# Performance work log

Measured on AMD Instinct MI355X. Metric: run time of the kernel, lower is better.

Reference implementation:

```python
import jax, jax.numpy as jnp
import numpy as np

N = 4096
D_IN = 1024
D_Q = 1024
D_V = 1024

def setup_inputs() -> dict:
    key = jax.random.key(0)
    ks = jax.random.split(key, 8)
    # x scaled down a bit so exp() of raw (unstable, no max-subtract) scores stays finite,
    # matching the original module's numerics regime.
    x = jax.random.normal(ks[0], (N, D_IN), dtype=jnp.float32) * 0.02
    mask = jax.random.uniform(ks[1], (N, N), dtype=jnp.float32)
    s = 1.0 / np.sqrt(D_IN)
    Wq = jax.random.normal(ks[2], (D_IN, D_Q), dtype=jnp.float32) * s
    bq = jax.random.normal(ks[3], (D_Q,), dtype=jnp.float32) * 0.02
    Wk = jax.random.normal(ks[4], (D_IN, D_Q), dtype=jnp.float32) * s
    bk = jax.random.normal(ks[5], (D_Q,), dtype=jnp.float32) * 0.02
    Wv = jax.random.normal(ks[6], (D_IN, D_V), dtype=jnp.float32) * s
    bv = jax.random.normal(ks[7], (D_V,), dtype=jnp.float32) * 0.02
    return {"x": x, "mask": mask, "Wq": Wq, "bq": bq, "Wk": Wk, "bk": bk, "Wv": Wv, "bv": bv}

def reference(x, mask, Wq, bq, Wk, bk, Wv, bv):
    # Q, K, V projections (nn.Linear: x @ W + b, here W stored as [in, out])
    Q = x @ Wq + bq          # [N, Dq]
    K = x @ Wk + bk          # [N, Dq]
    V = x @ Wv + bv          # [N, Dv]
    scale = 1.0              # default scale in original forward
    scores = scale * (Q @ K.T)   # [N, N]
    scores = mask * scores       # elementwise multiplicative mask
    # Faithful to original (quirky) normalization:
    # exp(S) / sum(exp(S), axis=1)[None, :]  -> row-sums broadcast across ROWS
    e = jnp.exp(scores)                       # [N, N]
    denom = jnp.sum(e, axis=1)[None, :]       # [1, N]
    softmax = e / denom                       # [N, N]
    return softmax @ V                        # [N, Dv]
```

## Files before the change

### kernel.cpp

```cpp
#include <hip/hip_runtime.h>
#include <hip/hip_bf16.h>


#define N_TOK 4096
#define D_DIM 1024

typedef __bf16 bf16x8 __attribute__((ext_vector_type(8)));
typedef __bf16 bf16x4 __attribute__((ext_vector_type(4)));
typedef float  f32x4  __attribute__((ext_vector_type(4)));

typedef const __attribute__((address_space(1))) char g_char;
typedef __attribute__((address_space(3))) char lds_char;

__global__ void cvt_f32_to_bf16(const float* __restrict__ in,
                                __bf16* __restrict__ out, int n) {
    int i = (blockIdx.x * 256 + threadIdx.x) * 4;
    if (i + 3 < n) {
        float4 v = *(const float4*)(in + i);
        bf16x4 o;
        o.x = (__bf16)v.x; o.y = (__bf16)v.y;
        o.z = (__bf16)v.z; o.w = (__bf16)v.w;
        *(bf16x4*)(out + i) = o;
    }
}

__global__ void transpose_w(const float* __restrict__ in, __bf16* __restrict__ outT) {
    __shared__ float t[64][65];
    const int c0 = blockIdx.x * 64, r0 = blockIdx.y * 64;
    const int tid = threadIdx.x;
#pragma unroll
    for (int k = 0; k < 16; k++) {
        int lin = tid + k * 256;
        int r = lin >> 6, c = lin & 63;
        t[r][c] = in[(size_t)(r0 + r) * 1024 + c0 + c];
    }
    __syncthreads();
#pragma unroll
    for (int k = 0; k < 16; k++) {
        int lin = tid + k * 256;
        int c = lin >> 6, r = lin & 63;
        outT[(size_t)(c0 + c) * 1024 + r0 + r] = (__bf16)t[r][c];
    }
}

__global__ void concat_bias(const float* __restrict__ bq, const float* __restrict__ bk,
                            const float* __restrict__ bv, float* __restrict__ bcat) {
    int i = blockIdx.x * 256 + threadIdx.x;
    if (i < 1024) bcat[i] = bq[i];
    else if (i < 2048) bcat[i] = bk[i - 1024];
    else if (i < 3072) bcat[i] = bv[i - 2048];
}

__global__ void rowsum_kernel(const __bf16* __restrict__ E, float* __restrict__ denom) {
    const int row = blockIdx.x;
    const int tid = threadIdx.x;
    const __bf16* p = E + (size_t)row * N_TOK + tid * 16;
    bf16x8 v0 = *(const bf16x8*)p;
    bf16x8 v1 = *(const bf16x8*)(p + 8);
    float s = 0.f;
#pragma unroll
    for (int i = 0; i < 8; i++) s += (float)v0[i] + (float)v1[i];
#pragma unroll
    for (int off = 32; off > 0; off >>= 1) s += __shfl_down(s, off, 64);
    __shared__ float partial[4];
    if ((tid & 63) == 0) partial[tid >> 6] = s;
    __syncthreads();
    if (tid == 0) denom[row] = partial[0] + partial[1] + partial[2] + partial[3];
}

__global__ void scale_transpose(const __bf16* __restrict__ V, int ldv,
                                const float* __restrict__ denom,
                                __bf16* __restrict__ VT) {
    __shared__ float t[64][65];
    __shared__ float rd[64];
    const int d0 = blockIdx.x * 64, j0 = blockIdx.y * 64;
    const int tid = threadIdx.x;
    if (tid < 64) rd[tid] = 1.0f / denom[j0 + tid];
    __syncthreads();
#pragma unroll
    for (int k = 0; k < 16; k++) {
        int lin = tid + k * 256;
        int j = lin >> 6, d = lin & 63;
        t[j][d] = (float)V[(size_t)(j0 + j) * ldv + d0 + d] * rd[j];
    }
    __syncthreads();
#pragma unroll
    for (int k = 0; k < 16; k++) {
        int lin = tid + k * 256;
        int d = lin >> 6, j = lin & 63;
        VT[(size_t)(d0 + d) * N_TOK + j0 + j] = (__bf16)t[j][d];
    }
}

__global__ void add_inplace(float* __restrict__ out, const float* __restrict__ p) {
    int i = (blockIdx.x * 256 + threadIdx.x) * 4;
    float4 a = *(const float4*)(out + i);
    float4 b = *(const float4*)(p + i);
    a.x += b.x; a.y += b.y; a.z += b.z; a.w += b.w;
    *(float4*)(out + i) = a;
}

template <int EPI>
__global__ __launch_bounds__(256, 2)
void gemm_nt(const __bf16* __restrict__ A, const __bf16* __restrict__ B,
             int lda, int ldb, int ldc, int Kz,
             const float* __restrict__ bias,
             const float* __restrict__ mask,
             __bf16* __restrict__ Cb,
             float* __restrict__ Cf0, float* __restrict__ Cf1) {
    __shared__ __bf16 lA[128 * 32];
    __shared__ __bf16 lB[128 * 32];

    const int tid  = threadIdx.x;
    const int wave = tid >> 6;
    const int lane = tid & 63;
    const int quad = lane >> 4;
    const int l16  = lane & 15;
    const int m0 = blockIdx.y * 128;
    const int n0 = blockIdx.x * 128;
    const int wr = (wave >> 1) * 64;
    const int wc = (wave & 1) * 64;

    const size_t lda_b = (size_t)lda * 2;
    const size_t ldb_b = (size_t)ldb * 2;
    const int o = tid * 16;
    const size_t koff = (size_t)blockIdx.z * Kz * 2;
    const char* gA = (const char*)A + (size_t)(m0 + (o >> 6)) * lda_b + (o & 63) + koff;
    const char* gB = (const char*)B + (size_t)(n0 + (o >> 6)) * ldb_b + (o & 63) + koff;
    const size_t cstepA = (size_t)64 * lda_b;
    const size_t cstepB = (size_t)64 * ldb_b;

    lds_char* lAp = (lds_char*)(void*)lA + wave * 1024;
    lds_char* lBp = (lds_char*)(void*)lB + wave * 1024;

    f32x4 acc[4][4];
#pragma unroll
    for (int i = 0; i < 4; i++)
#pragma unroll
        for (int j = 0; j < 4; j++) acc[i][j] = (f32x4){0.f, 0.f, 0.f, 0.f};

    for (int kt = 0; kt < Kz; kt += 32) {
        __builtin_amdgcn_global_load_lds((g_char*)gA,            lAp,        16, 0, 0);
        __builtin_amdgcn_global_load_lds((g_char*)(gA + cstepA), lAp + 4096, 16, 0, 0);
        __builtin_amdgcn_global_load_lds((g_char*)gB,            lBp,        16, 0, 0);
        __builtin_amdgcn_global_load_lds((g_char*)(gB + cstepB), lBp + 4096, 16, 0, 0);
        gA += 64;
        gB += 64;
        __syncthreads();

        bf16x8 af[4], bfr[4];
#pragma unroll
        for (int i = 0; i < 4; i++)
            af[i] = *(const bf16x8*)&lA[(wr + i * 16 + l16) * 32 + quad * 8];
#pragma unroll
        for (int i = 0; i < 4; i++)
            bfr[i] = *(const bf16x8*)&lB[(wc + i * 16 + l16) * 32 + quad * 8];

#pragma unroll
        for (int i = 0; i < 4; i++)
#pragma unroll
            for (int j = 0; j < 4; j++)
                acc[i][j] = __builtin_amdgcn_mfma_f32_16x16x32_bf16(
                    af[i], bfr[j], acc[i][j], 0, 0, 0);
        __syncthreads();
    }

    float* Cf = (blockIdx.z == 0) ? Cf0 : Cf1;

#pragma unroll
    for (int i = 0; i < 4; i++) {
#pragma unroll
        for (int j = 0; j < 4; j++) {
            const int col   = n0 + wc + j * 16 + l16;
            const int rbase = m0 + wr + i * 16 + quad * 4;
            f32x4 v = acc[i][j];
            if (EPI == 0) {
                const float bb = bias[col];
#pragma unroll
                for (int r = 0; r < 4; r++)
                    Cb[(size_t)(rbase + r) * ldc + col] = (__bf16)(v[r] + bb);
            } else if (EPI == 1) {
#pragma unroll
                for (int r = 0; r < 4; r++) {
                    size_t idx = (size_t)(rbase + r) * ldc + col;
                    Cb[idx] = (__bf16)__expf(mask[idx] * v[r]);
                }
            } else {
#pragma unroll
                for (int r = 0; r < 4; r++)
                    Cf[(size_t)(rbase + r) * ldc + col] = v[r];
            }
        }
    }
}

extern "C" void kernel_launch(void* const* d_in, const int* in_sizes, int n_in,
                              void* d_out, int out_size, void* d_ws, size_t ws_size,
                              hipStream_t stream) {
    const float* x    = (const float*)d_in[0];
    const float* mask = (const float*)d_in[1];
    const float* Wq   = (const float*)d_in[2];
    const float* bq   = (const float*)d_in[3];
    const float* Wk   = (const float*)d_in[4];
    const float* bk   = (const float*)d_in[5];
    const float* Wv   = (const float*)d_in[6];
    const float* bv   = (const float*)d_in[7];
    float* out = (float*)d_out;
    char* ws = (char*)d_ws;

    const size_t MB = 1024 * 1024;
    __bf16* Eb    = (__bf16*)(ws + 0 * MB);
    __bf16* QKVb  = (__bf16*)(ws + 32 * MB);
    float*  P1    = (float*)(ws + 32 * MB);
    __bf16* xb    = (__bf16*)(ws + 56 * MB);
    __bf16* VsT   = xb;
    __bf16* WcatT = (__bf16*)(ws + 64 * MB);
    float*  bcat  = (float*)(ws + 70 * MB);
    float*  denom = (float*)(ws + 70 * MB + 64 * 1024);

    cvt_f32_to_bf16<<<4096, 256, 0, stream>>>(x, xb, N_TOK * D_DIM);
    transpose_w<<<dim3(16, 16), 256, 0, stream>>>(Wq, WcatT);
    transpose_w<<<dim3(16, 16), 256, 0, stream>>>(Wk, WcatT + 1024 * 1024);
    transpose_w<<<dim3(16, 16), 256, 0, stream>>>(Wv, WcatT + 2048 * 1024);
    concat_bias<<<12, 256, 0, stream>>>(bq, bk, bv, bcat);

    gemm_nt<0><<<dim3(24, 32, 1), 256, 0, stream>>>(
        xb, WcatT, D_DIM, D_DIM, 3 * D_DIM, D_DIM,
        bcat, nullptr, QKVb, nullptr, nullptr);

    const __bf16* Qb = QKVb;
    const __bf16* Kb = QKVb + D_DIM;
    gemm_nt<1><<<dim3(32, 32, 1), 256, 0, stream>>>(
        Qb, Kb, 3 * D_DIM, 3 * D_DIM, N_TOK, D_DIM,
        nullptr, mask, Eb, nullptr, nullptr);

    rowsum_kernel<<<N_TOK, 256, 0, stream>>>(Eb, denom);

    scale_transpose<<<dim3(16, 64), 256, 0, stream>>>(QKVb + 2048, 3 * D_DIM, denom, VsT);

    gemm_nt<2><<<dim3(8, 32, 2), 256, 0, stream>>>(
        Eb, VsT, N_TOK, N_TOK, D_DIM, N_TOK / 2,
        nullptr, nullptr, nullptr, out, P1);

    add_inplace<<<4096, 256, 0, stream>>>(out, P1);
}
```

Measured before the change: 289.3 us.

## Fuse rowsum into exp GEMM, widen K-tile with swizzled LDS, drop split-K

Several changes land together. The row-sum of exp(scores) now happens inside the QK^T GEMM epilogue through shuffle reductions and atomicAdd into a zeroed denom buffer, and the separate rowsum kernel is removed. The GEMM now stages a 64-wide K tile in LDS with an XOR swizzle meant to avoid bank conflicts. The final E@V GEMM uses a 128x64 tile instead of split-K plus an add kernel. The setup kernels are also merged to cut launch count. The trade-offs are atomics contending on denom, float atomic ordering nondeterminism, and larger LDS use per block.

```diff
diff --git a/kernel.cpp b/kernel.cpp
--- a/kernel.cpp
+++ b/kernel.cpp
@@ -12,19 +12,29 @@
 typedef const __attribute__((address_space(1))) char g_char;
 typedef __attribute__((address_space(3))) char lds_char;
 
-__global__ void cvt_f32_to_bf16(const float* __restrict__ in,
-                                __bf16* __restrict__ out, int n) {
-    int i = (blockIdx.x * 256 + threadIdx.x) * 4;
-    if (i + 3 < n) {
-        float4 v = *(const float4*)(in + i);
+__global__ void cvt_and_bias(const float* __restrict__ x, __bf16* __restrict__ xb,
+                             const float* __restrict__ bq, const float* __restrict__ bk,
+                             const float* __restrict__ bv, float* __restrict__ bcat) {
+    int b = blockIdx.x;
+    if (b < 4096) {
+        int i = (b * 256 + threadIdx.x) * 4;
+        float4 v = *(const float4*)(x + i);
         bf16x4 o;
         o.x = (__bf16)v.x; o.y = (__bf16)v.y;
         o.z = (__bf16)v.z; o.w = (__bf16)v.w;
-        *(bf16x4*)(out + i) = o;
-    }
-}
-
-__global__ void transpose_w(const float* __restrict__ in, __bf16* __restrict__ outT) {
+        *(bf16x4*)(xb + i) = o;
+    } else {
+        int i = (b - 4096) * 256 + threadIdx.x;
+        if (i < 1024) bcat[i] = bq[i];
+        else if (i < 2048) bcat[i] = bk[i - 1024];
+        else if (i < 3072) bcat[i] = bv[i - 2048];
+    }
+}
+
+__global__ void transpose_w3(const float* __restrict__ Wq, const float* __restrict__ Wk,
+                             const float* __restrict__ Wv, __bf16* __restrict__ outT) {
+    const float* in = (blockIdx.z == 0) ? Wq : (blockIdx.z == 1) ? Wk : Wv;
+    __bf16* oT = outT + (size_t)blockIdx.z * 1024 * 1024;
     __shared__ float t[64][65];
     const int c0 = blockIdx.x * 64, r0 = blockIdx.y * 64;
     const int tid = threadIdx.x;
@@ -39,33 +49,8 @@
     for (int k = 0; k < 16; k++) {
         int lin = tid + k * 256;
         int c = lin >> 6, r = lin & 63;
-        outT[(size_t)(c0 + c) * 1024 + r0 + r] = (__bf16)t[r][c];
-    }
-}
-
-__global__ void concat_bias(const float* __restrict__ bq, const float* __restrict__ bk,
-                            const float* __restrict__ bv, float* __restrict__ bcat) {
-    int i = blockIdx.x * 256 + threadIdx.x;
-    if (i < 1024) bcat[i] = bq[i];
-    else if (i < 2048) bcat[i] = bk[i - 1024];
-    else if (i < 3072) bcat[i] = bv[i - 2048];
-}
-
-__global__ void rowsum_kernel(const __bf16* __restrict__ E, float* __restrict__ denom) {
-    const int row = blockIdx.x;
-    const int tid = threadIdx.x;
-    const __bf16* p = E + (size_t)row * N_TOK + tid * 16;
-    bf16x8 v0 = *(const bf16x8*)p;
-    bf16x8 v1 = *(const bf16x8*)(p + 8);
-    float s = 0.f;
-#pragma unroll
-    for (int i = 0; i < 8; i++) s += (float)v0[i] + (float)v1[i];
-#pragma unroll
-    for (int off = 32; off > 0; off >>= 1) s += __shfl_down(s, off, 64);
-    __shared__ float partial[4];
-    if ((tid & 63) == 0) partial[tid >> 6] = s;
-    __syncthreads();
-    if (tid == 0) denom[row] = partial[0] + partial[1] + partial[2] + partial[3];
+        oT[(size_t)(c0 + c) * 1024 + r0 + r] = (__bf16)t[r][c];
+    }
 }
 
 __global__ void scale_transpose(const __bf16* __restrict__ V, int ldv,
@@ -92,24 +77,17 @@
     }
 }
 
-__global__ void add_inplace(float* __restrict__ out, const float* __restrict__ p) {
-    int i = (blockIdx.x * 256 + threadIdx.x) * 4;
-    float4 a = *(const float4*)(out + i);
-    float4 b = *(const float4*)(p + i);
-    a.x += b.x; a.y += b.y; a.z += b.z; a.w += b.w;
-    *(float4*)(out + i) = a;
-}
-
-template <int EPI>
+template <int EPI, int TN>
 __global__ __launch_bounds__(256, 2)
 void gemm_nt(const __bf16* __restrict__ A, const __bf16* __restrict__ B,
-             int lda, int ldb, int ldc, int Kz,
+             int lda, int ldb, int ldc, int K,
              const float* __restrict__ bias,
              const float* __restrict__ mask,
-             __bf16* __restrict__ Cb,
-             float* __restrict__ Cf0, float* __restrict__ Cf1) {
-    __shared__ __bf16 lA[128 * 32];
-    __shared__ __bf16 lB[128 * 32];
+             __bf16* __restrict__ Cb, float* __restrict__ Cf,
+             float* __restrict__ denom) {
+    constexpr int NF = TN / 32;
+    __shared__ __bf16 lA[128 * 64];
+    __shared__ __bf16 lB[TN * 64];
 
     const int tid  = threadIdx.x;
     const int wave = tid >> 6;
@@ -117,62 +95,78 @@
     const int quad = lane >> 4;
     const int l16  = lane & 15;
     const int m0 = blockIdx.y * 128;
-    const int n0 = blockIdx.x * 128;
+    const int n0 = blockIdx.x * TN;
     const int wr = (wave >> 1) * 64;
-    const int wc = (wave & 1) * 64;
+    const int wc = (wave & 1) * (TN / 2);
 
     const size_t lda_b = (size_t)lda * 2;
     const size_t ldb_b = (size_t)ldb * 2;
-    const int o = tid * 16;
-    const size_t koff = (size_t)blockIdx.z * Kz * 2;
-    const char* gA = (const char*)A + (size_t)(m0 + (o >> 6)) * lda_b + (o & 63) + koff;
-    const char* gB = (const char*)B + (size_t)(n0 + (o >> 6)) * ldb_b + (o & 63) + koff;
-    const size_t cstepA = (size_t)64 * lda_b;
-    const size_t cstepB = (size_t)64 * ldb_b;
+    const int tr = tid >> 3;
+    const int ts = ((tid & 7) ^ (tr & 7)) * 16;
+    const char* gA = (const char*)A + (size_t)(m0 + tr) * lda_b + ts;
+    const char* gB = (const char*)B + (size_t)(n0 + tr) * ldb_b + ts;
+    const size_t pstepA = (size_t)32 * lda_b;
+    const size_t pstepB = (size_t)32 * ldb_b;
 
     lds_char* lAp = (lds_char*)(void*)lA + wave * 1024;
     lds_char* lBp = (lds_char*)(void*)lB + wave * 1024;
 
-    f32x4 acc[4][4];
+    const int l7 = l16 & 7;
+    const int rdA0 = ((wr + l16) * 128 + ((quad ^ l7) * 16)) >> 1;
+    const int rdA1 = ((wr + l16) * 128 + (((4 + quad) ^ l7) * 16)) >> 1;
+    const int rdB0 = ((wc + l16) * 128 + ((quad ^ l7) * 16)) >> 1;
+    const int rdB1 = ((wc + l16) * 128 + (((4 + quad) ^ l7) * 16)) >> 1;
+
+    f32x4 acc[4][NF];
 #pragma unroll
     for (int i = 0; i < 4; i++)
 #pragma unroll
-        for (int j = 0; j < 4; j++) acc[i][j] = (f32x4){0.f, 0.f, 0.f, 0.f};
-
-    for (int kt = 0; kt < Kz; kt += 32) {
-        __builtin_amdgcn_global_load_lds((g_char*)gA,            lAp,        16, 0, 0);
-        __builtin_amdgcn_global_load_lds((g_char*)(gA + cstepA), lAp + 4096, 16, 0, 0);
-        __builtin_amdgcn_global_load_lds((g_char*)gB,            lBp,        16, 0, 0);
-        __builtin_amdgcn_global_load_lds((g_char*)(gB + cstepB), lBp + 4096, 16, 0, 0);
-        gA += 64;
-        gB += 64;
+        for (int j = 0; j < NF; j++) acc[i][j] = (f32x4){0.f, 0.f, 0.f, 0.f};
+
+    for (int kt = 0; kt < K; kt += 64) {
+#pragma unroll
+        for (int c = 0; c < 4; c++)
+            __builtin_amdgcn_global_load_lds((g_char*)(gA + c * pstepA),
+                                             lAp + c * 4096, 16, 0, 0);
+#pragma unroll
+        for (int c = 0; c < NF; c++)
+            __builtin_amdgcn_global_load_lds((g_char*)(gB + c * pstepB),
+                                             lBp + c * 4096, 16, 0, 0);
+        gA += 128;
+        gB += 128;
         __syncthreads();
 
-        bf16x8 af[4], bfr[4];
+        bf16x8 af[4], bfr[NF];
+#pragma unroll
+        for (int i = 0; i < 4; i++) af[i] = *(const bf16x8*)&lA[rdA0 + i * 1024];
+#pragma unroll
+        for (int j = 0; j < NF; j++) bfr[j] = *(const bf16x8*)&lB[rdB0 + j * 1024];
 #pragma unroll
         for (int i = 0; i < 4; i++)
-            af[i] = *(const bf16x8*)&lA[(wr + i * 16 + l16) * 32 + quad * 8];
+#pragma unroll
+            for (int j = 0; j < NF; j++)
+                acc[i][j] = __builtin_amdgcn_mfma_f32_16x16x32_bf16(
+                    af[i], bfr[j], acc[i][j], 0, 0, 0);
+#pragma unroll
+        for (int i = 0; i < 4; i++) af[i] = *(const bf16x8*)&lA[rdA1 + i * 1024];
+#pragma unroll
+        for (int j = 0; j < NF; j++) bfr[j] = *(const bf16x8*)&lB[rdB1 + j * 1024];
 #pragma unroll
         for (int i = 0; i < 4; i++)
-            bfr[i] = *(const bf16x8*)&lB[(wc + i * 16 + l16) * 32 + quad * 8];
-
-#pragma unroll
-        for (int i = 0; i < 4; i++)
-#pragma unroll
-            for (int j = 0; j < 4; j++)
+#pragma unroll
+            for (int j = 0; j < NF; j++)
                 acc[i][j] = __builtin_amdgcn_mfma_f32_16x16x32_bf16(
                     af[i], bfr[j], acc[i][j], 0, 0, 0);
         __syncthreads();
     }
 
-    float* Cf = (blockIdx.z == 0) ? Cf0 : Cf1;
-
 #pragma unroll
     for (int i = 0; i < 4; i++) {
-#pragma unroll
-        for (int j = 0; j < 4; j++) {
-            const int col   = n0 + wc + j * 16 + l16;
-            const int rbase = m0 + wr + i * 16 + quad * 4;
+        const int rbase = m0 + wr + i * 16 + quad * 4;
+        f32x4 rs = (f32x4){0.f, 0.f, 0.f, 0.f};
+#pragma unroll
+        for (int j = 0; j < NF; j++) {
+            const int col = n0 + wc + j * 16 + l16;
             f32x4 v = acc[i][j];
             if (EPI == 0) {
                 const float bb = bias[col];
@@ -183,12 +177,25 @@
 #pragma unroll
                 for (int r = 0; r < 4; r++) {
                     size_t idx = (size_t)(rbase + r) * ldc + col;
-                    Cb[idx] = (__bf16)__expf(mask[idx] * v[r]);
+                    __bf16 eb = (__bf16)__expf(mask[idx] * v[r]);
+                    Cb[idx] = eb;
+                    rs[r] += (float)eb;
                 }
             } else {
 #pragma unroll
                 for (int r = 0; r < 4; r++)
                     Cf[(size_t)(rbase + r) * ldc + col] = v[r];
+            }
+        }
+        if (EPI == 1) {
+#pragma unroll
+            for (int m = 1; m < 16; m <<= 1) {
+#pragma unroll
+                for (int r = 0; r < 4; r++) rs[r] += __shfl_xor(rs[r], m, 64);
+            }
+            if (l16 == 0) {
+#pragma unroll
+                for (int r = 0; r < 4; r++) atomicAdd(&denom[rbase + r], rs[r]);
             }
         }
     }
@@ -211,36 +218,30 @@
     const size_t MB = 1024 * 1024;
     __bf16* Eb    = (__bf16*)(ws + 0 * MB);
     __bf16* QKVb  = (__bf16*)(ws + 32 * MB);
-    float*  P1    = (float*)(ws + 32 * MB);
     __bf16* xb    = (__bf16*)(ws + 56 * MB);
     __bf16* VsT   = xb;
     __bf16* WcatT = (__bf16*)(ws + 64 * MB);
     float*  bcat  = (float*)(ws + 70 * MB);
     float*  denom = (float*)(ws + 70 * MB + 64 * 1024);
 
-    cvt_f32_to_bf16<<<4096, 256, 0, stream>>>(x, xb, N_TOK * D_DIM);
-    transpose_w<<<dim3(16, 16), 256, 0, stream>>>(Wq, WcatT);
-    transpose_w<<<dim3(16, 16), 256, 0, stream>>>(Wk, WcatT + 1024 * 1024);
-    transpose_w<<<dim3(16, 16), 256, 0, stream>>>(Wv, WcatT + 2048 * 1024);
-    concat_bias<<<12, 256, 0, stream>>>(bq, bk, bv, bcat);
-
-    gemm_nt<0><<<dim3(24, 32, 1), 256, 0, stream>>>(
+    hipMemsetAsync(denom, 0, N_TOK * sizeof(float), stream);
+
+    cvt_and_bias<<<4096 + 12, 256, 0, stream>>>(x, xb, bq, bk, bv, bcat);
+    transpose_w3<<<dim3(16, 16, 3), 256, 0, stream>>>(Wq, Wk, Wv, WcatT);
+
+    gemm_nt<0, 128><<<dim3(24, 32), 256, 0, stream>>>(
         xb, WcatT, D_DIM, D_DIM, 3 * D_DIM, D_DIM,
         bcat, nullptr, QKVb, nullptr, nullptr);
 
     const __bf16* Qb = QKVb;
     const __bf16* Kb = QKVb + D_DIM;
-    gemm_nt<1><<<dim3(32, 32, 1), 256, 0, stream>>>(
+    gemm_nt<1, 128><<<dim3(32, 32), 256, 0, stream>>>(
         Qb, Kb, 3 * D_DIM, 3 * D_DIM, N_TOK, D_DIM,
-        nullptr, mask, Eb, nullptr, nullptr);
-
-    rowsum_kernel<<<N_TOK, 256, 0, stream>>>(Eb, denom);
+        nullptr, mask, Eb, nullptr, denom);
 
     scale_transpose<<<dim3(16, 64), 256, 0, stream>>>(QKVb + 2048, 3 * D_DIM, denom, VsT);
 
-    gemm_nt<2><<<dim3(8, 32, 2), 256, 0, stream>>>(
-        Eb, VsT, N_TOK, N_TOK, D_DIM, N_TOK / 2,
-        nullptr, nullptr, nullptr, out, P1);
-
-    add_inplace<<<4096, 256, 0, stream>>>(out, P1);
-}
+    gemm_nt<2, 64><<<dim3(16, 32), 256, 0, stream>>>(
+        Eb, VsT, N_TOK, N_TOK, D_DIM, N_TOK,
+        nullptr, nullptr, nullptr, out, nullptr);
+}
```

New measurement: 261.3 us. 9.7% less time.
